# Kernel tuning notes

Hardware: AMD Instinct MI355X
Metric: run time of the kernel (lower is better)

Reference implementation:

```python
import jax, jax.numpy as jnp
import numpy as np

B, S, D = 4, 2048, 1024
N_EXPERTS, EXPERT_SIZE = 16, 256
WIDTH = N_EXPERTS * EXPERT_SIZE  # 4096


def setup_inputs() -> dict:
    key = jax.random.key(0)
    k_x, k_w1, k_w2, k_g = jax.random.split(key, 4)
    x = jax.random.normal(k_x, (B, S, D), dtype=jnp.float32)
    # Linear params, fan-in scaled init
    w1 = jax.random.normal(k_w1, (D, WIDTH), dtype=jnp.float32) / np.sqrt(D).astype(np.float32)
    b1 = jnp.zeros((WIDTH,), dtype=jnp.float32)
    w2 = jax.random.normal(k_w2, (WIDTH, D), dtype=jnp.float32) / np.sqrt(WIDTH).astype(np.float32)
    b2 = jnp.zeros((D,), dtype=jnp.float32)
    return {"x": x, "w1": w1, "b1": b1, "w2": w2, "b2": b2}


def reference(x, w1, b1, w2, b2):
    # NOTE: the original module computes expert-choice routing tensors
    # (gate einsum -> topk -> one_hot -> identity matmul 'gather'), but the
    # returned value is ONLY the dense FFN applied to x; all routing results
    # are dead code with no effect on the output. Faithful output math:
    h = jax.nn.relu(jnp.einsum('bsd,dw->bsw', x, w1) + b1)  # [B,S,WIDTH]
    return jnp.einsum('bsw,wd->bsd', h, w2) + b2            # [B,S,D]
```

## Files before the change

kernel.cpp:

```cpp
#include <hip/hip_runtime.h>
#include <hip/hip_bf16.h>


typedef __bf16 bf16;
typedef __bf16 bf16x4 __attribute__((ext_vector_type(4)));
typedef __bf16 bf16x8 __attribute__((ext_vector_type(8)));
typedef float  f32x4  __attribute__((ext_vector_type(4)));

#define BM 128
#define BN 128
#define BK 64

__device__ __forceinline__ void gload_lds16(const bf16* g, bf16* l) {
    __builtin_amdgcn_global_load_lds(
        (const __attribute__((address_space(1))) unsigned int*)g,
        (__attribute__((address_space(3))) unsigned int*)l,
        16, 0, 0);
}

__global__ __launch_bounds__(256) void cast_f32_bf16(
    const float4* __restrict__ in, bf16x4* __restrict__ out, int n4)
{
    int i = blockIdx.x * 256 + threadIdx.x;
    if (i < n4) {
        float4 v = in[i];
        bf16x4 o;
        o.x = (bf16)v.x; o.y = (bf16)v.y; o.z = (bf16)v.z; o.w = (bf16)v.w;
        out[i] = o;
    }
}

__global__ __launch_bounds__(256) void transpose_cast(
    const float* __restrict__ in, bf16* __restrict__ out, int K, int N)
{
    __shared__ __align__(16) bf16 tile[64][72];
    const int k0 = blockIdx.y * 64;
    const int n0 = blockIdx.x * 64;
    const int t  = threadIdx.x;

    const int lr = t >> 4;
    const int lc = (t & 15) << 2;
#pragma unroll
    for (int p = 0; p < 4; ++p) {
        int k = p * 16 + lr;
        float4 v = *(const float4*)(in + (size_t)(k0 + k) * N + n0 + lc);
        tile[lc + 0][k] = (bf16)v.x;
        tile[lc + 1][k] = (bf16)v.y;
        tile[lc + 2][k] = (bf16)v.z;
        tile[lc + 3][k] = (bf16)v.w;
    }
    __syncthreads();

    const int wr = t >> 3;
    const int wc = (t & 7) << 3;
#pragma unroll
    for (int p = 0; p < 2; ++p) {
        int n = p * 32 + wr;
        *(bf16x8*)(out + (size_t)(n0 + n) * K + k0 + wc) =
            *(const bf16x8*)&tile[n][wc];
    }
}

template <int FUSE_RELU_BF16>
__global__ __launch_bounds__(256, 3) void gemm_bt(
    const bf16* __restrict__ A, const bf16* __restrict__ Bt,
    const float* __restrict__ bias, void* __restrict__ Cout,
    int M, int N, int K)
{
    __shared__ __align__(16) bf16 As[BM * BK];
    __shared__ __align__(16) bf16 Bs[BN * BK];

    const int tid  = threadIdx.x;
    const int wave = tid >> 6;
    const int lane = tid & 63;

    const int l8  = lane >> 3;
    const int c8  = lane & 7;
    const int swc = (c8 ^ l8) << 3;
    const size_t K_ = (size_t)K;

    const bf16* gA[4]; const bf16* gB[4];
    bf16* lA[4]; bf16* lB[4];
#pragma unroll
    for (int g = 0; g < 4; ++g) {
        const int rr = wave * 32 + g * 8 + l8;
        gA[g] = A  + ((size_t)blockIdx.y * BM + rr) * K_ + swc;
        gB[g] = Bt + ((size_t)blockIdx.x * BN + rr) * K_ + swc;
        lA[g] = &As[(wave * 32 + g * 8) * BK] + lane * 8;
        lB[g] = &Bs[(wave * 32 + g * 8) * BK] + lane * 8;
    }

    const int wm   = (wave >> 1) << 6;
    const int wn   = (wave & 1) << 6;
    const int quad = lane >> 4;
    const int r    = lane & 15;
    const int r7   = lane & 7;

    f32x4 acc[4][4] = {};

    for (int k0 = 0; k0 < K; k0 += BK) {
        __syncthreads();
#pragma unroll
        for (int g = 0; g < 4; ++g) {
            gload_lds16(gA[g], lA[g]);
            gload_lds16(gB[g], lB[g]);
            gA[g] += BK; gB[g] += BK;
        }
        __syncthreads();

#pragma unroll
        for (int h = 0; h < 2; ++h) {
            const int ch = ((h * 4 + quad) ^ r7) << 3;
            bf16x8 af[4], bfr[4];
#pragma unroll
            for (int i = 0; i < 4; ++i)
                af[i] = *(const bf16x8*)&As[(wm + i * 16 + r) * BK + ch];
#pragma unroll
            for (int j = 0; j < 4; ++j)
                bfr[j] = *(const bf16x8*)&Bs[(wn + j * 16 + r) * BK + ch];
#pragma unroll
            for (int i = 0; i < 4; ++i)
#pragma unroll
                for (int j = 0; j < 4; ++j)
                    acc[i][j] = __builtin_amdgcn_mfma_f32_16x16x32_bf16(
                        af[i], bfr[j], acc[i][j], 0, 0, 0);
        }
    }

    const int m_base = blockIdx.y * BM + wm + quad * 4;
    const int n_base = blockIdx.x * BN + wn + r;
    float bv[4];
#pragma unroll
    for (int j = 0; j < 4; ++j) bv[j] = bias[n_base + j * 16];

    if (FUSE_RELU_BF16) {
        bf16* Cb = (bf16*)Cout;
#pragma unroll
        for (int i = 0; i < 4; ++i) {
#pragma unroll
            for (int p = 0; p < 4; ++p) {
                size_t row = (size_t)(m_base + i * 16 + p) * (size_t)N;
#pragma unroll
                for (int j = 0; j < 4; ++j) {
                    float v = acc[i][j][p] + bv[j];
                    v = v > 0.f ? v : 0.f;
                    Cb[row + n_base + j * 16] = (bf16)v;
                }
            }
        }
    } else {
        float* Cf = (float*)Cout;
#pragma unroll
        for (int i = 0; i < 4; ++i) {
#pragma unroll
            for (int p = 0; p < 4; ++p) {
                size_t row = (size_t)(m_base + i * 16 + p) * (size_t)N;
#pragma unroll
                for (int j = 0; j < 4; ++j) {
                    Cf[row + n_base + j * 16] = acc[i][j][p] + bv[j];
                }
            }
        }
    }
}

extern "C" void kernel_launch(void* const* d_in, const int* in_sizes, int n_in,
                              void* d_out, int out_size, void* d_ws, size_t ws_size,
                              hipStream_t stream)
{
    const float* x  = (const float*)d_in[0];
    const float* w1 = (const float*)d_in[1];
    const float* b1 = (const float*)d_in[2];
    const float* w2 = (const float*)d_in[3];
    const float* b2 = (const float*)d_in[4];
    float* out = (float*)d_out;

    const int M = 8192, D = 1024, W = 4096;

    char* ws = (char*)d_ws;
    bf16* xb  = (bf16*)(ws);
    bf16* w1t = (bf16*)(ws + (size_t)(16 << 20));
    bf16* w2t = (bf16*)(ws + (size_t)(24 << 20));
    bf16* h   = (bf16*)(ws + (size_t)(32 << 20));

    {
        int n4 = (M * D) / 4;
        cast_f32_bf16<<<(n4 + 255) / 256, 256, 0, stream>>>(
            (const float4*)x, (bf16x4*)xb, n4);
    }
    transpose_cast<<<dim3(W / 64, D / 64), 256, 0, stream>>>(w1, w1t, D, W);
    transpose_cast<<<dim3(D / 64, W / 64), 256, 0, stream>>>(w2, w2t, W, D);

    gemm_bt<1><<<dim3(W / BN, M / BM), 256, 0, stream>>>(
        xb, w1t, b1, (void*)h, M, W, D);

    gemm_bt<0><<<dim3(D / BN, M / BM), 256, 0, stream>>>(
        h, w2t, b2, (void*)out, M, D, W);
}
```

Before: 252.0 us.

## Triple-buffer GEMM mainloop with 256x128 tiles, 512 threads, XCD-aware block remap

```diff
diff --git a/kernel.cpp b/kernel.cpp
--- a/kernel.cpp
+++ b/kernel.cpp
@@ -7,7 +7,7 @@
 typedef __bf16 bf16x8 __attribute__((ext_vector_type(8)));
 typedef float  f32x4  __attribute__((ext_vector_type(4)));
 
-#define BM 128
+#define BM 256
 #define BN 128
 #define BK 64
 
@@ -62,32 +62,39 @@
 }
 
 template <int FUSE_RELU_BF16>
-__global__ __launch_bounds__(256, 3) void gemm_bt(
+__global__ __launch_bounds__(512, 2) void gemm_bt(
     const bf16* __restrict__ A, const bf16* __restrict__ Bt,
     const float* __restrict__ bias, void* __restrict__ Cout,
-    int M, int N, int K)
-{
-    __shared__ __align__(16) bf16 As[BM * BK];
-    __shared__ __align__(16) bf16 Bs[BN * BK];
+    int M, int N, int K, int ny)
+{
+    __shared__ __align__(16) bf16 As[3 * BM * BK];
+    __shared__ __align__(16) bf16 Bs[3 * BN * BK];
+
+    const int nwg = gridDim.x;
+    const int bid = blockIdx.x;
+    const int L   = (bid & 7) * (nwg >> 3) + (bid >> 3);
+    const int tx  = L / ny;
+    const int ty  = L - tx * ny;
 
     const int tid  = threadIdx.x;
     const int wave = tid >> 6;
     const int lane = tid & 63;
-
-    const int l8  = lane >> 3;
-    const int c8  = lane & 7;
-    const int swc = (c8 ^ l8) << 3;
+    const int l8   = lane >> 3;
+    const int c8   = lane & 7;
+    const int swc  = (c8 ^ l8) << 3;
     const size_t K_ = (size_t)K;
 
-    const bf16* gA[4]; const bf16* gB[4];
-    bf16* lA[4]; bf16* lB[4];
-#pragma unroll
-    for (int g = 0; g < 4; ++g) {
-        const int rr = wave * 32 + g * 8 + l8;
-        gA[g] = A  + ((size_t)blockIdx.y * BM + rr) * K_ + swc;
-        gB[g] = Bt + ((size_t)blockIdx.x * BN + rr) * K_ + swc;
-        lA[g] = &As[(wave * 32 + g * 8) * BK] + lane * 8;
-        lB[g] = &Bs[(wave * 32 + g * 8) * BK] + lane * 8;
+    const bf16* gA_s[4]; const bf16* gB_s[2];
+    int ldsAo[4], ldsBo[2];
+#pragma unroll
+    for (int j = 0; j < 4; ++j) {
+        gA_s[j]  = A + ((size_t)ty * BM + j * 64 + wave * 8 + l8) * K_ + swc;
+        ldsAo[j] = (j * 64 + wave * 8) * BK + lane * 8;
+    }
+#pragma unroll
+    for (int j = 0; j < 2; ++j) {
+        gB_s[j]  = Bt + ((size_t)tx * BN + j * 64 + wave * 8 + l8) * K_ + swc;
+        ldsBo[j] = (j * 64 + wave * 8) * BK + lane * 8;
     }
 
     const int wm   = (wave >> 1) << 6;
@@ -96,39 +103,119 @@
     const int r    = lane & 15;
     const int r7   = lane & 7;
 
+    const int NT = K >> 6;
+
+#pragma unroll
+    for (int j = 0; j < 4; ++j) gload_lds16(gA_s[j], As + ldsAo[j]);
+#pragma unroll
+    for (int j = 0; j < 2; ++j) gload_lds16(gB_s[j], Bs + ldsBo[j]);
+#pragma unroll
+    for (int j = 0; j < 4; ++j) gA_s[j] += BK;
+#pragma unroll
+    for (int j = 0; j < 2; ++j) gB_s[j] += BK;
+#pragma unroll
+    for (int j = 0; j < 4; ++j) gload_lds16(gA_s[j], As + BM * BK + ldsAo[j]);
+#pragma unroll
+    for (int j = 0; j < 2; ++j) gload_lds16(gB_s[j], Bs + BN * BK + ldsBo[j]);
+#pragma unroll
+    for (int j = 0; j < 4; ++j) gA_s[j] += BK;
+#pragma unroll
+    for (int j = 0; j < 2; ++j) gB_s[j] += BK;
+
+    asm volatile("s_waitcnt vmcnt(6)" ::: "memory");
+    __builtin_amdgcn_s_barrier();
+    asm volatile("" ::: "memory");
+
     f32x4 acc[4][4] = {};
-
-    for (int k0 = 0; k0 < K; k0 += BK) {
-        __syncthreads();
-#pragma unroll
-        for (int g = 0; g < 4; ++g) {
-            gload_lds16(gA[g], lA[g]);
-            gload_lds16(gB[g], lB[g]);
-            gA[g] += BK; gB[g] += BK;
-        }
-        __syncthreads();
-
-#pragma unroll
-        for (int h = 0; h < 2; ++h) {
-            const int ch = ((h * 4 + quad) ^ r7) << 3;
-            bf16x8 af[4], bfr[4];
-#pragma unroll
-            for (int i = 0; i < 4; ++i)
-                af[i] = *(const bf16x8*)&As[(wm + i * 16 + r) * BK + ch];
-#pragma unroll
-            for (int j = 0; j < 4; ++j)
-                bfr[j] = *(const bf16x8*)&Bs[(wn + j * 16 + r) * BK + ch];
-#pragma unroll
-            for (int i = 0; i < 4; ++i)
-#pragma unroll
-                for (int j = 0; j < 4; ++j)
-                    acc[i][j] = __builtin_amdgcn_mfma_f32_16x16x32_bf16(
-                        af[i], bfr[j], acc[i][j], 0, 0, 0);
-        }
-    }
-
-    const int m_base = blockIdx.y * BM + wm + quad * 4;
-    const int n_base = blockIdx.x * BN + wn + r;
+    int bc = 0;
+
+    for (int t = 0; t < NT; ++t) {
+        const int bn  = bc ? bc - 1 : 2;
+        const int bcA = bc * (BM * BK), bcB = bc * (BN * BK);
+        const int bnA = bn * (BM * BK), bnB = bn * (BN * BK);
+        const bool do_stage = (t + 2 < NT);
+
+        bf16x8 af[4][2], bb[2][2];
+#pragma unroll
+        for (int i = 0; i < 4; ++i)
+#pragma unroll
+            for (int h = 0; h < 2; ++h)
+                af[i][h] = *(const bf16x8*)&As[bcA + (wm + i * 16 + r) * BK +
+                                              (((h * 4 + quad) ^ r7) << 3)];
+#pragma unroll
+        for (int j = 0; j < 2; ++j)
+#pragma unroll
+            for (int h = 0; h < 2; ++h)
+                bb[j][h] = *(const bf16x8*)&Bs[bcB + (wn + j * 16 + r) * BK +
+                                               (((h * 4 + quad) ^ r7) << 3)];
+        if (do_stage) {
+            gload_lds16(gA_s[0], As + bnA + ldsAo[0]);
+            gload_lds16(gA_s[1], As + bnA + ldsAo[1]);
+            gload_lds16(gA_s[2], As + bnA + ldsAo[2]);
+        }
+
+        asm volatile("" ::: "memory");
+        __builtin_amdgcn_s_barrier();
+        asm volatile("s_waitcnt lgkmcnt(0)" ::: "memory");
+        __builtin_amdgcn_sched_barrier(0);
+        __builtin_amdgcn_s_setprio(1);
+#pragma unroll
+        for (int i = 0; i < 4; ++i)
+#pragma unroll
+            for (int j = 0; j < 2; ++j) {
+                acc[i][j] = __builtin_amdgcn_mfma_f32_16x16x32_bf16(
+                    af[i][0], bb[j][0], acc[i][j], 0, 0, 0);
+                acc[i][j] = __builtin_amdgcn_mfma_f32_16x16x32_bf16(
+                    af[i][1], bb[j][1], acc[i][j], 0, 0, 0);
+            }
+        __builtin_amdgcn_s_setprio(0);
+        asm volatile("" ::: "memory");
+        __builtin_amdgcn_s_barrier();
+        asm volatile("" ::: "memory");
+
+        bf16x8 bb2[2][2];
+#pragma unroll
+        for (int j = 0; j < 2; ++j)
+#pragma unroll
+            for (int h = 0; h < 2; ++h)
+                bb2[j][h] = *(const bf16x8*)&Bs[bcB + (wn + (j + 2) * 16 + r) * BK +
+                                                (((h * 4 + quad) ^ r7) << 3)];
+        if (do_stage) {
+            gload_lds16(gA_s[3], As + bnA + ldsAo[3]);
+            gload_lds16(gB_s[0], Bs + bnB + ldsBo[0]);
+            gload_lds16(gB_s[1], Bs + bnB + ldsBo[1]);
+#pragma unroll
+            for (int j = 0; j < 4; ++j) gA_s[j] += BK;
+#pragma unroll
+            for (int j = 0; j < 2; ++j) gB_s[j] += BK;
+        }
+
+        asm volatile("" ::: "memory");
+        __builtin_amdgcn_s_barrier();
+        asm volatile("s_waitcnt lgkmcnt(0)" ::: "memory");
+        __builtin_amdgcn_sched_barrier(0);
+        __builtin_amdgcn_s_setprio(1);
+#pragma unroll
+        for (int i = 0; i < 4; ++i)
+#pragma unroll
+            for (int j = 0; j < 2; ++j) {
+                acc[i][j + 2] = __builtin_amdgcn_mfma_f32_16x16x32_bf16(
+                    af[i][0], bb2[j][0], acc[i][j + 2], 0, 0, 0);
+                acc[i][j + 2] = __builtin_amdgcn_mfma_f32_16x16x32_bf16(
+                    af[i][1], bb2[j][1], acc[i][j + 2], 0, 0, 0);
+            }
+        __builtin_amdgcn_s_setprio(0);
+
+        if (do_stage)        { asm volatile("s_waitcnt vmcnt(6)" ::: "memory"); }
+        else if (t + 1 < NT) { asm volatile("s_waitcnt vmcnt(0)" ::: "memory"); }
+        __builtin_amdgcn_s_barrier();
+        asm volatile("" ::: "memory");
+
+        bc = (bc == 2) ? 0 : bc + 1;
+    }
+
+    const int m_base = ty * BM + wm + quad * 4;
+    const int n_base = tx * BN + wn + r;
     float bv[4];
 #pragma unroll
     for (int j = 0; j < 4; ++j) bv[j] = bias[n_base + j * 16];
@@ -191,9 +278,12 @@
     transpose_cast<<<dim3(W / 64, D / 64), 256, 0, stream>>>(w1, w1t, D, W);
     transpose_cast<<<dim3(D / 64, W / 64), 256, 0, stream>>>(w2, w2t, W, D);
 
-    gemm_bt<1><<<dim3(W / BN, M / BM), 256, 0, stream>>>(
-        xb, w1t, b1, (void*)h, M, W, D);
-
-    gemm_bt<0><<<dim3(D / BN, M / BM), 256, 0, stream>>>(
-        h, w2t, b2, (void*)out, M, D, W);
-}
+    {
+        int ny = M / BM, nwg = (W / BN) * ny;
+        gemm_bt<1><<<nwg, 512, 0, stream>>>(xb, w1t, b1, (void*)h, M, W, D, ny);
+    }
+    {
+        int ny = M / BM, nwg = (D / BN) * ny;
+        gemm_bt<0><<<nwg, 512, 0, stream>>>(h, w2t, b2, (void*)out, M, D, W, ny);
+    }
+}
```

New measurement: 299.6 us. 1.19x slower.

## Switch GEMM to 32x32x16 MFMA tiles and fuse prep kernels into one launch

Applied to the files above, without the earlier changes.

```diff
diff --git a/kernel.cpp b/kernel.cpp
--- a/kernel.cpp
+++ b/kernel.cpp
@@ -5,7 +5,7 @@
 typedef __bf16 bf16;
 typedef __bf16 bf16x4 __attribute__((ext_vector_type(4)));
 typedef __bf16 bf16x8 __attribute__((ext_vector_type(8)));
-typedef float  f32x4  __attribute__((ext_vector_type(4)));
+typedef float  f32x16 __attribute__((ext_vector_type(16)));
 
 #define BM 128
 #define BN 128
@@ -18,26 +18,10 @@
         16, 0, 0);
 }
 
-__global__ __launch_bounds__(256) void cast_f32_bf16(
-    const float4* __restrict__ in, bf16x4* __restrict__ out, int n4)
+__device__ __forceinline__ void transpose_tile(
+    const float* __restrict__ in, bf16* __restrict__ out,
+    int K, int N, int k0, int n0, int t, bf16 (*tile)[72])
 {
-    int i = blockIdx.x * 256 + threadIdx.x;
-    if (i < n4) {
-        float4 v = in[i];
-        bf16x4 o;
-        o.x = (bf16)v.x; o.y = (bf16)v.y; o.z = (bf16)v.z; o.w = (bf16)v.w;
-        out[i] = o;
-    }
-}
-
-__global__ __launch_bounds__(256) void transpose_cast(
-    const float* __restrict__ in, bf16* __restrict__ out, int K, int N)
-{
-    __shared__ __align__(16) bf16 tile[64][72];
-    const int k0 = blockIdx.y * 64;
-    const int n0 = blockIdx.x * 64;
-    const int t  = threadIdx.x;
-
     const int lr = t >> 4;
     const int lc = (t & 15) << 2;
 #pragma unroll
@@ -61,6 +45,30 @@
     }
 }
 
+__global__ __launch_bounds__(256) void prep_fused(
+    const float* __restrict__ x,  bf16* __restrict__ xb,
+    const float* __restrict__ w1, bf16* __restrict__ w1t,
+    const float* __restrict__ w2, bf16* __restrict__ w2t)
+{
+    __shared__ __align__(16) bf16 tile[64][72];
+    const int bid = blockIdx.x;
+    const int t   = threadIdx.x;
+
+    if (bid < 8192) {
+        int i = bid * 256 + t;
+        float4 v = ((const float4*)x)[i];
+        bf16x4 o;
+        o.x = (bf16)v.x; o.y = (bf16)v.y; o.z = (bf16)v.z; o.w = (bf16)v.w;
+        ((bf16x4*)xb)[i] = o;
+    } else if (bid < 9216) {
+        int b = bid - 8192;
+        transpose_tile(w1, w1t, 1024, 4096, (b >> 6) * 64, (b & 63) * 64, t, tile);
+    } else {
+        int b = bid - 9216;
+        transpose_tile(w2, w2t, 4096, 1024, (b >> 4) * 64, (b & 15) * 64, t, tile);
+    }
+}
+
 template <int FUSE_RELU_BF16>
 __global__ __launch_bounds__(256, 3) void gemm_bt(
     const bf16* __restrict__ A, const bf16* __restrict__ Bt,
@@ -69,6 +77,9 @@
 {
     __shared__ __align__(16) bf16 As[BM * BK];
     __shared__ __align__(16) bf16 Bs[BN * BK];
+
+    const int tx = blockIdx.x;
+    const int ty = blockIdx.y;
 
     const int tid  = threadIdx.x;
     const int wave = tid >> 6;
@@ -84,19 +95,19 @@
 #pragma unroll
     for (int g = 0; g < 4; ++g) {
         const int rr = wave * 32 + g * 8 + l8;
-        gA[g] = A  + ((size_t)blockIdx.y * BM + rr) * K_ + swc;
-        gB[g] = Bt + ((size_t)blockIdx.x * BN + rr) * K_ + swc;
+        gA[g] = A  + ((size_t)ty * BM + rr) * K_ + swc;
+        gB[g] = Bt + ((size_t)tx * BN + rr) * K_ + swc;
         lA[g] = &As[(wave * 32 + g * 8) * BK] + lane * 8;
         lB[g] = &Bs[(wave * 32 + g * 8) * BK] + lane * 8;
     }
 
-    const int wm   = (wave >> 1) << 6;
-    const int wn   = (wave & 1) << 6;
-    const int quad = lane >> 4;
-    const int r    = lane & 15;
-    const int r7   = lane & 7;
+    const int wm  = (wave >> 1) << 6;
+    const int wn  = (wave & 1) << 6;
+    const int c31 = lane & 31;
+    const int kh  = lane >> 5;
+    const int r7  = lane & 7;
 
-    f32x4 acc[4][4] = {};
+    f32x16 acc[2][2] = {};
 
     for (int k0 = 0; k0 < K; k0 += BK) {
         __syncthreads();
@@ -109,55 +120,50 @@
         __syncthreads();
 
 #pragma unroll
-        for (int h = 0; h < 2; ++h) {
-            const int ch = ((h * 4 + quad) ^ r7) << 3;
-            bf16x8 af[4], bfr[4];
-#pragma unroll
-            for (int i = 0; i < 4; ++i)
-                af[i] = *(const bf16x8*)&As[(wm + i * 16 + r) * BK + ch];
-#pragma unroll
-            for (int j = 0; j < 4; ++j)
-                bfr[j] = *(const bf16x8*)&Bs[(wn + j * 16 + r) * BK + ch];
-#pragma unroll
-            for (int i = 0; i < 4; ++i)
-#pragma unroll
-                for (int j = 0; j < 4; ++j)
-                    acc[i][j] = __builtin_amdgcn_mfma_f32_16x16x32_bf16(
-                        af[i], bfr[j], acc[i][j], 0, 0, 0);
+        for (int c = 0; c < 4; ++c) {
+            const int ch = ((2 * c + kh) ^ r7) << 3;
+            bf16x8 a0 = *(const bf16x8*)&As[(wm +      c31) * BK + ch];
+            bf16x8 a1 = *(const bf16x8*)&As[(wm + 32 + c31) * BK + ch];
+            bf16x8 b0 = *(const bf16x8*)&Bs[(wn +      c31) * BK + ch];
+            bf16x8 b1 = *(const bf16x8*)&Bs[(wn + 32 + c31) * BK + ch];
+            acc[0][0] = __builtin_amdgcn_mfma_f32_32x32x16_bf16(a0, b0, acc[0][0], 0, 0, 0);
+            acc[0][1] = __builtin_amdgcn_mfma_f32_32x32x16_bf16(a0, b1, acc[0][1], 0, 0, 0);
+            acc[1][0] = __builtin_amdgcn_mfma_f32_32x32x16_bf16(a1, b0, acc[1][0], 0, 0, 0);
+            acc[1][1] = __builtin_amdgcn_mfma_f32_32x32x16_bf16(a1, b1, acc[1][1], 0, 0, 0);
         }
     }
 
-    const int m_base = blockIdx.y * BM + wm + quad * 4;
-    const int n_base = blockIdx.x * BN + wn + r;
-    float bv[4];
+    const int m_base = ty * BM + wm + 4 * kh;
+    const int n_base = tx * BN + wn + c31;
+    float bv[2];
 #pragma unroll
-    for (int j = 0; j < 4; ++j) bv[j] = bias[n_base + j * 16];
+    for (int j = 0; j < 2; ++j) bv[j] = bias[n_base + j * 32];
 
     if (FUSE_RELU_BF16) {
         bf16* Cb = (bf16*)Cout;
 #pragma unroll
-        for (int i = 0; i < 4; ++i) {
+        for (int i = 0; i < 2; ++i) {
 #pragma unroll
-            for (int p = 0; p < 4; ++p) {
-                size_t row = (size_t)(m_base + i * 16 + p) * (size_t)N;
+            for (int reg = 0; reg < 16; ++reg) {
+                size_t row = (size_t)(m_base + i * 32 + (reg & 3) + 8 * (reg >> 2)) * (size_t)N;
 #pragma unroll
-                for (int j = 0; j < 4; ++j) {
-                    float v = acc[i][j][p] + bv[j];
+                for (int j = 0; j < 2; ++j) {
+                    float v = acc[i][j][reg] + bv[j];
                     v = v > 0.f ? v : 0.f;
-                    Cb[row + n_base + j * 16] = (bf16)v;
+                    Cb[row + n_base + j * 32] = (bf16)v;
                 }
             }
         }
     } else {
         float* Cf = (float*)Cout;
 #pragma unroll
-        for (int i = 0; i < 4; ++i) {
+        for (int i = 0; i < 2; ++i) {
 #pragma unroll
-            for (int p = 0; p < 4; ++p) {
-                size_t row = (size_t)(m_base + i * 16 + p) * (size_t)N;
+            for (int reg = 0; reg < 16; ++reg) {
+                size_t row = (size_t)(m_base + i * 32 + (reg & 3) + 8 * (reg >> 2)) * (size_t)N;
 #pragma unroll
-                for (int j = 0; j < 4; ++j) {
-                    Cf[row + n_base + j * 16] = acc[i][j][p] + bv[j];
+                for (int j = 0; j < 2; ++j) {
+                    Cf[row + n_base + j * 32] = acc[i][j][reg] + bv[j];
                 }
             }
         }
@@ -183,13 +189,7 @@
     bf16* w2t = (bf16*)(ws + (size_t)(24 << 20));
     bf16* h   = (bf16*)(ws + (size_t)(32 << 20));
 
-    {
-        int n4 = (M * D) / 4;
-        cast_f32_bf16<<<(n4 + 255) / 256, 256, 0, stream>>>(
-            (const float4*)x, (bf16x4*)xb, n4);
-    }
-    transpose_cast<<<dim3(W / 64, D / 64), 256, 0, stream>>>(w1, w1t, D, W);
-    transpose_cast<<<dim3(D / 64, W / 64), 256, 0, stream>>>(w2, w2t, W, D);
+    prep_fused<<<10240, 256, 0, stream>>>(x, xb, w1, w1t, w2, w2t);
 
     gemm_bt<1><<<dim3(W / BN, M / BM), 256, 0, stream>>>(
         xb, w1t, b1, (void*)h, M, W, D);
```

Measured after the change: 263.1 us. 4.4% more time.
